# Optimization experiments

Hardware: AMD Instinct MI355X
Metric: run time of the kernel (lower is better)

Reference implementation:

```python
import jax, jax.numpy as jnp
import numpy as np

SEQ, BATCH, HIDDEN = 4096, 16, 512


def setup_inputs() -> dict:
    key = jax.random.key(0)
    ks = jax.random.split(key, 8)
    scale = 1.0 / np.sqrt(HIDDEN)
    outputs_hidden = jax.random.normal(ks[0], (1, BATCH, HIDDEN), jnp.float32)
    encoder_out = jax.random.normal(ks[1], (SEQ, BATCH, HIDDEN), jnp.float32)
    encoder_features = jax.random.normal(ks[2], (SEQ, BATCH, HIDDEN), jnp.float32)
    # binary-ish float mask, mostly ones
    encoder_mask = (jax.random.uniform(ks[3], (BATCH, 1, SEQ)) > 0.1).astype(jnp.float32)
    # running sum of positive exp-scores; keep strictly positive
    temporal_scores_sum = jax.random.uniform(ks[4], (BATCH, 1, SEQ)) + 0.5
    W_feat = jax.random.normal(ks[5], (HIDDEN, HIDDEN), jnp.float32) * scale
    b_feat = jax.random.normal(ks[6], (HIDDEN,), jnp.float32)
    v_attn = jax.random.normal(ks[7], (HIDDEN,), jnp.float32) * scale
    return {
        "outputs_hidden": outputs_hidden,
        "encoder_out": encoder_out,
        "encoder_features": encoder_features,
        "encoder_mask": encoder_mask,
        "temporal_scores_sum": temporal_scores_sum,
        "W_feat": W_feat,
        "b_feat": b_feat,
        "v_attn": v_attn,
    }


def reference(outputs_hidden, encoder_out, encoder_features, encoder_mask,
              temporal_scores_sum, W_feat, b_feat, v_attn):
    # self.features: Linear(hidden, hidden) on decoder state [1, b, h]
    decoder_features = jnp.einsum('obh,kh->obk', outputs_hidden, W_feat) + b_feat
    # additive score: tanh(dec + enc) . v  -> [s, b]
    scores = jnp.einsum('sbh,h->sb', jnp.tanh(decoder_features + encoder_features), v_attn)
    # Permute(1,2,0) of [s,b,1] -> [b,1,s], then exp
    temporal_attention = jnp.exp(scores).T[:, None, :]  # [b, 1, s]
    attention = temporal_attention / temporal_scores_sum
    new_scores_sum = temporal_attention + temporal_scores_sum
    attention = attention * encoder_mask
    attention = attention / jnp.sum(attention, axis=-1, keepdims=True)  # Normalize(-1)
    enc = jnp.transpose(encoder_out, (1, 0, 2))           # [b, s, h]
    context = jnp.matmul(attention, enc)                  # [b, 1, h]
    context = jnp.transpose(context, (1, 0, 2))           # [1, b, h]
    return context, attention, new_scores_sum
```

## Files before the change

### kernel.cpp

```cpp
#include <hip/hip_runtime.h>
#include <hip/hip_bf16.h>
#include <stdint.h>

#define SEQ 4096
#define BATCH 16
#define HID 512
#define ATT_OFF (BATCH * HID)
#define NSS_OFF (BATCH * HID + BATCH * SEQ)

typedef unsigned short u16;
typedef unsigned int u32;

__device__ __forceinline__ float bflo(u32 w) { return __uint_as_float(w << 16); }
__device__ __forceinline__ float bfhi(u32 w) { return __uint_as_float(w & 0xffff0000u); }

__device__ __forceinline__ u16 f2bf(float f) {
  u32 u = __float_as_uint(f);
  return (u16)((u + 0x7fffu + ((u >> 16) & 1u)) >> 16);
}

__device__ __forceinline__ int probe_bf16(const void* tssp) {
  const u16* t = (const u16*)tssp;
  int ok = 1;
  #pragma unroll
  for (int i = 0; i < 8; i += 2) {
    u16 u = t[i];
    ok &= (u >= 0x3F00 && u <= 0x3FC0) ? 1 : 0;
  }
  return ok;
}

template <int BF>
__device__ __forceinline__ float ld1(const void* p, size_t i) {
  if (BF) return __uint_as_float(((u32)((const u16*)p)[i]) << 16);
  return ((const float*)p)[i];
}

template <int BF>
__device__ __forceinline__ void st1(void* p, size_t i, float v) {
  if (BF) ((u16*)p)[i] = f2bf(v);
  else    ((float*)p)[i] = v;
}

template <int BF>
__device__ __forceinline__ void load8(const void* p, size_t e, float* o) {
  if (BF) {
    uint4 v = *(const uint4*)((const u16*)p + e);
    o[0]=bflo(v.x); o[1]=bfhi(v.x); o[2]=bflo(v.y); o[3]=bfhi(v.y);
    o[4]=bflo(v.z); o[5]=bfhi(v.z); o[6]=bflo(v.w); o[7]=bfhi(v.w);
  } else {
    const float4* f = (const float4*)((const float*)p + e);
    float4 a = f[0], b = f[1];
    o[0]=a.x; o[1]=a.y; o[2]=a.z; o[3]=a.w;
    o[4]=b.x; o[5]=b.y; o[6]=b.z; o[7]=b.w;
  }
}

__device__ __forceinline__ float fast_tanh(float x) {
  float e = __expf(2.0f * x);
  return 1.0f - 2.0f * __builtin_amdgcn_rcpf(e + 1.0f);
}

__device__ __forceinline__ float wave_sum(float acc) {
  #pragma unroll
  for (int off = 32; off; off >>= 1) acc += __shfl_xor(acc, off, 64);
  return acc;
}

template <int BF>
__device__ __forceinline__ void k_dec_body(
    const void* oh, const void* W, const void* bias, float* dec) {
  int tid = threadIdx.x;
  int gw = blockIdx.x * 4 + (tid >> 6);
  int lane = tid & 63;
  int k = gw & (HID - 1);
  int b = gw >> 9;
  float wv[8], ov[8];
  load8<BF>(W,  (size_t)k * HID + lane * 8, wv);
  load8<BF>(oh, (size_t)b * HID + lane * 8, ov);
  float acc = 0.0f;
  #pragma unroll
  for (int j = 0; j < 8; ++j) acc += wv[j] * ov[j];
  acc = wave_sum(acc);
  if (lane == 0) dec[b * HID + k] = acc + ld1<BF>(bias, k);
}

__global__ __launch_bounds__(256) void k_dec(
    const void* oh, const void* W, const void* bias, const void* tss,
    float* dec, float* denom) {
  if (blockIdx.x == 0 && threadIdx.x < BATCH) denom[threadIdx.x] = 0.0f;
  if (probe_bf16(tss)) k_dec_body<1>(oh, W, bias, dec);
  else                 k_dec_body<0>(oh, W, bias, dec);
}

template <int BF>
__device__ __forceinline__ void k_scores_body(
    const void* ef, const void* maskp, const void* tssp, const void* vp,
    const float* dec, float* w_out, float* denom, void* out) {
  int tid = threadIdx.x, lane = tid & 63, wave = tid >> 6;
  int blk = blockIdx.x;
  int b = blk >> 8;
  int s_base = (blk & 255) * 16;
  float dv[8], vv[8];
  #pragma unroll
  for (int j = 0; j < 8; ++j) dv[j] = dec[b * HID + lane * 8 + j];
  load8<BF>(vp, lane * 8, vv);
  __shared__ float wpart[16];
  #pragma unroll
  for (int i = 0; i < 4; ++i) {
    int s = s_base + wave * 4 + i;
    float ev[8];
    load8<BF>(ef, ((size_t)s * BATCH + b) * HID + lane * 8, ev);
    float acc = 0.0f;
    #pragma unroll
    for (int j = 0; j < 8; ++j) acc += fast_tanh(ev[j] + dv[j]) * vv[j];
    acc = wave_sum(acc);
    if (lane == 0) {
      float p  = __expf(acc);
      float ts = ld1<BF>(tssp,  b * SEQ + s);
      float m  = ld1<BF>(maskp, b * SEQ + s);
      float w  = p * m * __builtin_amdgcn_rcpf(ts);
      st1<BF>(out, NSS_OFF + b * SEQ + s, p + ts);
      w_out[b * SEQ + s] = w;
      wpart[wave * 4 + i] = w;
    }
  }
  __syncthreads();
  if (tid == 0) {
    float sum = 0.0f;
    #pragma unroll
    for (int j = 0; j < 16; ++j) sum += wpart[j];
    atomicAdd(&denom[b], sum);
  }
}

__global__ __launch_bounds__(256) void k_scores(
    const void* ef, const void* maskp, const void* tssp, const void* vp,
    const float* dec, float* w_out, float* denom, void* out) {
  if (probe_bf16(tssp)) k_scores_body<1>(ef, maskp, tssp, vp, dec, w_out, denom, out);
  else                  k_scores_body<0>(ef, maskp, tssp, vp, dec, w_out, denom, out);
}

#define K3_CHUNK 128
template <int BF>
__device__ __forceinline__ void k_context_body(
    const void* eo, const float* w, const float* denom,
    float* partial, void* out) {
  int blk = blockIdx.x;
  int b = blk >> 5;
  int chunk = blk & 31;
  int s0 = chunk * K3_CHUNK;
  int tid = threadIdx.x, lane = tid & 63, sg = tid >> 6;
  __shared__ float w_s[K3_CHUNK];
  __shared__ float red[192 * 8];
  float inv_d = __builtin_amdgcn_rcpf(denom[b]);
  if (tid < K3_CHUNK) {
    float wv = w[b * SEQ + s0 + tid];
    w_s[tid] = wv;
    st1<BF>(out, ATT_OFF + b * SEQ + s0 + tid, wv * inv_d);
  }
  __syncthreads();
  float a[8] = {0,0,0,0,0,0,0,0};
  #pragma unroll 4
  for (int i = 0; i < K3_CHUNK / 4; ++i) {
    int sl = 4 * i + sg;
    int s = s0 + sl;
    float ev[8];
    load8<BF>(eo, ((size_t)s * BATCH + b) * HID + lane * 8, ev);
    float ws = w_s[sl];
    #pragma unroll
    for (int j = 0; j < 8; ++j) a[j] += ws * ev[j];
  }
  if (sg > 0) {
    float* r = &red[(((sg - 1) * 64) + lane) * 8];
    #pragma unroll
    for (int j = 0; j < 8; ++j) r[j] = a[j];
  }
  __syncthreads();
  if (sg == 0) {
    #pragma unroll
    for (int k = 0; k < 3; ++k) {
      const float* r = &red[((k * 64) + lane) * 8];
      #pragma unroll
      for (int j = 0; j < 8; ++j) a[j] += r[j];
    }
    float4* p4 = (float4*)(partial + (size_t)chunk * (BATCH * HID) + b * HID + lane * 8);
    p4[0] = make_float4(a[0], a[1], a[2], a[3]);
    p4[1] = make_float4(a[4], a[5], a[6], a[7]);
  }
}

__global__ __launch_bounds__(256) void k_context(
    const void* eo, const float* w, const float* denom, const void* tssp,
    float* partial, void* out) {
  if (probe_bf16(tssp)) k_context_body<1>(eo, w, denom, partial, out);
  else                  k_context_body<0>(eo, w, denom, partial, out);
}

__global__ __launch_bounds__(256) void k_reduce_ctx(
    const float* __restrict__ partial, const float* __restrict__ denom,
    const void* tssp, void* out) {
  int idx = blockIdx.x * 256 + threadIdx.x;
  int b = idx >> 9;
  float sum = 0.0f;
  #pragma unroll
  for (int c = 0; c < 32; ++c) sum += partial[c * (BATCH * HID) + idx];
  float v = sum * __builtin_amdgcn_rcpf(denom[b]);
  if (probe_bf16(tssp)) st1<1>(out, idx, v);
  else                  st1<0>(out, idx, v);
}

extern "C" void kernel_launch(void* const* d_in, const int* in_sizes, int n_in,
                              void* d_out, int out_size, void* d_ws, size_t ws_size,
                              hipStream_t stream) {
  const void* oh   = d_in[0];
  const void* eo   = d_in[1];
  const void* ef   = d_in[2];
  const void* mask = d_in[3];
  const void* tss  = d_in[4];
  const void* W    = d_in[5];
  const void* bias = d_in[6];
  const void* v    = d_in[7];

  float* ws      = (float*)d_ws;
  float* dec     = ws;
  float* w_buf   = dec + BATCH * HID;
  float* denom   = w_buf + BATCH * SEQ;
  float* partial = denom + 16;

  k_dec       <<<2048, 256, 0, stream>>>(oh, W, bias, tss, dec, denom);
  k_scores    <<<4096, 256, 0, stream>>>(ef, mask, tss, v, dec, w_buf, denom, d_out);
  k_context   <<< 512, 256, 0, stream>>>(eo, w_buf, denom, tss, partial, d_out);
  k_reduce_ctx<<<  32, 256, 0, stream>>>(partial, denom, tss, d_out);
}
```

Measured before the change: 322.3 us.

## Fuse score and context passes into one kernel with unnormalized accumulation

Scores and the weighted context sum now run in one kernel that reads encoder_features and encoder_out rows together. Each block accumulates the unnormalized weighted sum over a 64-row chunk, and a small finalize kernel divides by the denominator and writes both the attention and context outputs. This removes one kernel launch and the separate pass that re-read the weights, leaving one streaming pass over both large tensors. The trade-offs are fewer blocks (1024) with a serial 16-step loop per wave, and a finalize that runs on only 16 blocks and loops over 64 partials per element.

```diff
diff --git a/kernel.cpp b/kernel.cpp
--- a/kernel.cpp
+++ b/kernel.cpp
@@ -7,6 +7,9 @@
 #define HID 512
 #define ATT_OFF (BATCH * HID)
 #define NSS_OFF (BATCH * HID + BATCH * SEQ)
+#define SPB 64
+#define NCHUNK (SEQ / SPB)
+#define SPW (SPB / 4)
 
 typedef unsigned short u16;
 typedef unsigned int u32;
@@ -94,120 +97,104 @@
 }
 
 template <int BF>
-__device__ __forceinline__ void k_scores_body(
-    const void* ef, const void* maskp, const void* tssp, const void* vp,
-    const float* dec, float* w_out, float* denom, void* out) {
+__device__ __forceinline__ void k_fused_body(
+    const void* ef, const void* eo, const void* maskp, const void* tssp,
+    const void* vp, const float* dec, float* w_buf, float* denom,
+    float* partial, void* out) {
   int tid = threadIdx.x, lane = tid & 63, wave = tid >> 6;
   int blk = blockIdx.x;
-  int b = blk >> 8;
-  int s_base = (blk & 255) * 16;
+  int b = blk >> 6;
+  int chunk = blk & (NCHUNK - 1);
+  int s0 = chunk * SPB + wave * SPW;
   float dv[8], vv[8];
   #pragma unroll
   for (int j = 0; j < 8; ++j) dv[j] = dec[b * HID + lane * 8 + j];
   load8<BF>(vp, lane * 8, vv);
-  __shared__ float wpart[16];
-  #pragma unroll
-  for (int i = 0; i < 4; ++i) {
-    int s = s_base + wave * 4 + i;
+  float a[8] = {0,0,0,0,0,0,0,0};
+  float wsum = 0.0f;
+  for (int i = 0; i < SPW; ++i) {
+    int s = s0 + i;
+    size_t rowoff = ((size_t)s * BATCH + b) * HID + lane * 8;
     float ev[8];
-    load8<BF>(ef, ((size_t)s * BATCH + b) * HID + lane * 8, ev);
+    load8<BF>(ef, rowoff, ev);
+    float eov[8];
+    load8<BF>(eo, rowoff, eov);
     float acc = 0.0f;
     #pragma unroll
     for (int j = 0; j < 8; ++j) acc += fast_tanh(ev[j] + dv[j]) * vv[j];
     acc = wave_sum(acc);
+    float p  = __expf(acc);
+    float ts = ld1<BF>(tssp,  b * SEQ + s);
+    float m  = ld1<BF>(maskp, b * SEQ + s);
+    float w  = p * m * __builtin_amdgcn_rcpf(ts);
     if (lane == 0) {
-      float p  = __expf(acc);
-      float ts = ld1<BF>(tssp,  b * SEQ + s);
-      float m  = ld1<BF>(maskp, b * SEQ + s);
-      float w  = p * m * __builtin_amdgcn_rcpf(ts);
       st1<BF>(out, NSS_OFF + b * SEQ + s, p + ts);
-      w_out[b * SEQ + s] = w;
-      wpart[wave * 4 + i] = w;
+      w_buf[b * SEQ + s] = w;
+      wsum += w;
     }
+    #pragma unroll
+    for (int j = 0; j < 8; ++j) a[j] += w * eov[j];
+  }
+  __shared__ float red[3 * 64 * 8];
+  __shared__ float wpart[4];
+  if (lane == 0) wpart[wave] = wsum;
+  if (wave > 0) {
+    float* r = &red[(((wave - 1) * 64) + lane) * 8];
+    #pragma unroll
+    for (int j = 0; j < 8; ++j) r[j] = a[j];
   }
   __syncthreads();
-  if (tid == 0) {
-    float sum = 0.0f;
-    #pragma unroll
-    for (int j = 0; j < 16; ++j) sum += wpart[j];
-    atomicAdd(&denom[b], sum);
-  }
-}
-
-__global__ __launch_bounds__(256) void k_scores(
-    const void* ef, const void* maskp, const void* tssp, const void* vp,
-    const float* dec, float* w_out, float* denom, void* out) {
-  if (probe_bf16(tssp)) k_scores_body<1>(ef, maskp, tssp, vp, dec, w_out, denom, out);
-  else                  k_scores_body<0>(ef, maskp, tssp, vp, dec, w_out, denom, out);
-}
-
-#define K3_CHUNK 128
-template <int BF>
-__device__ __forceinline__ void k_context_body(
-    const void* eo, const float* w, const float* denom,
-    float* partial, void* out) {
-  int blk = blockIdx.x;
-  int b = blk >> 5;
-  int chunk = blk & 31;
-  int s0 = chunk * K3_CHUNK;
-  int tid = threadIdx.x, lane = tid & 63, sg = tid >> 6;
-  __shared__ float w_s[K3_CHUNK];
-  __shared__ float red[192 * 8];
-  float inv_d = __builtin_amdgcn_rcpf(denom[b]);
-  if (tid < K3_CHUNK) {
-    float wv = w[b * SEQ + s0 + tid];
-    w_s[tid] = wv;
-    st1<BF>(out, ATT_OFF + b * SEQ + s0 + tid, wv * inv_d);
-  }
-  __syncthreads();
-  float a[8] = {0,0,0,0,0,0,0,0};
-  #pragma unroll 4
-  for (int i = 0; i < K3_CHUNK / 4; ++i) {
-    int sl = 4 * i + sg;
-    int s = s0 + sl;
-    float ev[8];
-    load8<BF>(eo, ((size_t)s * BATCH + b) * HID + lane * 8, ev);
-    float ws = w_s[sl];
-    #pragma unroll
-    for (int j = 0; j < 8; ++j) a[j] += ws * ev[j];
-  }
-  if (sg > 0) {
-    float* r = &red[(((sg - 1) * 64) + lane) * 8];
-    #pragma unroll
-    for (int j = 0; j < 8; ++j) r[j] = a[j];
-  }
-  __syncthreads();
-  if (sg == 0) {
+  if (wave == 0) {
     #pragma unroll
     for (int k = 0; k < 3; ++k) {
       const float* r = &red[((k * 64) + lane) * 8];
       #pragma unroll
       for (int j = 0; j < 8; ++j) a[j] += r[j];
     }
-    float4* p4 = (float4*)(partial + (size_t)chunk * (BATCH * HID) + b * HID + lane * 8);
+    float4* p4 = (float4*)(partial + ((size_t)b * NCHUNK + chunk) * HID + lane * 8);
     p4[0] = make_float4(a[0], a[1], a[2], a[3]);
     p4[1] = make_float4(a[4], a[5], a[6], a[7]);
-  }
-}
-
-__global__ __launch_bounds__(256) void k_context(
-    const void* eo, const float* w, const float* denom, const void* tssp,
+    if (tid == 0)
+      atomicAdd(&denom[b], wpart[0] + wpart[1] + wpart[2] + wpart[3]);
+  }
+}
+
+__global__ __launch_bounds__(256) void k_fused(
+    const void* ef, const void* eo, const void* maskp, const void* tssp,
+    const void* vp, const float* dec, float* w_buf, float* denom,
     float* partial, void* out) {
-  if (probe_bf16(tssp)) k_context_body<1>(eo, w, denom, partial, out);
-  else                  k_context_body<0>(eo, w, denom, partial, out);
-}
-
-__global__ __launch_bounds__(256) void k_reduce_ctx(
-    const float* __restrict__ partial, const float* __restrict__ denom,
+  if (probe_bf16(tssp))
+    k_fused_body<1>(ef, eo, maskp, tssp, vp, dec, w_buf, denom, partial, out);
+  else
+    k_fused_body<0>(ef, eo, maskp, tssp, vp, dec, w_buf, denom, partial, out);
+}
+
+template <int BF>
+__device__ __forceinline__ void k_fin_body(
+    const float* w_buf, const float* denom, const float* partial, void* out) {
+  int b = blockIdx.x;
+  int tid = threadIdx.x;
+  float inv_d = __builtin_amdgcn_rcpf(denom[b]);
+  #pragma unroll
+  for (int k = 0; k < SEQ / 256; ++k) {
+    int s = k * 256 + tid;
+    st1<BF>(out, ATT_OFF + b * SEQ + s, w_buf[b * SEQ + s] * inv_d);
+  }
+  #pragma unroll
+  for (int r = 0; r < HID / 256; ++r) {
+    int h = r * 256 + tid;
+    float sum = 0.0f;
+    for (int c = 0; c < NCHUNK; ++c)
+      sum += partial[((size_t)b * NCHUNK + c) * HID + h];
+    st1<BF>(out, b * HID + h, sum * inv_d);
+  }
+}
+
+__global__ __launch_bounds__(256) void k_finalize(
+    const float* w_buf, const float* denom, const float* partial,
     const void* tssp, void* out) {
-  int idx = blockIdx.x * 256 + threadIdx.x;
-  int b = idx >> 9;
-  float sum = 0.0f;
-  #pragma unroll
-  for (int c = 0; c < 32; ++c) sum += partial[c * (BATCH * HID) + idx];
-  float v = sum * __builtin_amdgcn_rcpf(denom[b]);
-  if (probe_bf16(tssp)) st1<1>(out, idx, v);
-  else                  st1<0>(out, idx, v);
+  if (probe_bf16(tssp)) k_fin_body<1>(w_buf, denom, partial, out);
+  else                  k_fin_body<0>(w_buf, denom, partial, out);
 }
 
 extern "C" void kernel_launch(void* const* d_in, const int* in_sizes, int n_in,
@@ -228,8 +215,8 @@
   float* denom   = w_buf + BATCH * SEQ;
   float* partial = denom + 16;
 
-  k_dec       <<<2048, 256, 0, stream>>>(oh, W, bias, tss, dec, denom);
-  k_scores    <<<4096, 256, 0, stream>>>(ef, mask, tss, v, dec, w_buf, denom, d_out);
-  k_context   <<< 512, 256, 0, stream>>>(eo, w_buf, denom, tss, partial, d_out);
-  k_reduce_ctx<<<  32, 256, 0, stream>>>(partial, denom, tss, d_out);
-}
+  k_dec     <<<2048, 256, 0, stream>>>(oh, W, bias, tss, dec, denom);
+  k_fused   <<<1024, 256, 0, stream>>>(ef, eo, mask, tss, v, dec, w_buf,
+                                       denom, partial, d_out);
+  k_finalize<<<  16, 256, 0, stream>>>(w_buf, denom, partial, tss, d_out);
+}
```

Result: faster. 308.2 us (-4.4%).
